# Performance work log

Hardware: AMD Instinct MI355X
Metric: run time of the kernel (lower is better)

Reference implementation:

```python
import jax, jax.numpy as jnp
import numpy as np

N = 50000   # nodes
E = 400000  # edges
F = 128     # in_channels == heads*out_channels (H*C)
H = 8       # heads
C = 16      # per-head out_channels (hidden_channels)
ED = 16     # edge_dim
G = 64      # num graphs in batch
OUT = 64    # encoder out_channels
NEG = 0.2   # leaky_relu negative slope
EPS = 1e-5  # batchnorm eps


def setup_inputs() -> dict:
    key = jax.random.key(0)
    ks = jax.random.split(key, 16)
    s = 0.09  # ~xavier scale for fan_in 128
    return {
        "x": jax.random.normal(ks[0], (N, F), jnp.float32),
        "edge_index": jax.random.randint(ks[1], (2, E), 0, N, dtype=jnp.int32),
        "edge_attr": jax.random.normal(ks[2], (E, ED), jnp.float32),
        "batch": jnp.sort(jax.random.randint(ks[3], (N,), 0, G, dtype=jnp.int32)),
        "lin_qkv": jax.random.normal(ks[4], (3, 3, F, F), jnp.float32) * s,   # [layer, q/k/v, out, in]
        "lin_edge": jax.random.normal(ks[5], (3, F, ED), jnp.float32) * s,    # [layer, out, edge_dim]
        "att": jax.random.normal(ks[6], (3, 3, H, C), jnp.float32) * 0.1,     # [layer, att_q/att_k/att_edge, H, C]
        "gat_bias": jnp.zeros((3, F), jnp.float32),
        "bn_scale": jnp.ones((3, F), jnp.float32),
        "bn_bias": jnp.zeros((3, F), jnp.float32),
        "W1": jax.random.normal(ks[7], (64, 128), jnp.float32) * s,
        "b1": jnp.zeros((64,), jnp.float32),
        "bn1_s": jnp.ones((64,), jnp.float32),
        "bn1_b": jnp.zeros((64,), jnp.float32),
        "W2": jax.random.normal(ks[8], (32, 64), jnp.float32) * 0.12,
        "b2": jnp.zeros((32,), jnp.float32),
        "bn2_s": jnp.ones((32,), jnp.float32),
        "bn2_b": jnp.zeros((32,), jnp.float32),
        "Wout": jax.random.normal(ks[9], (OUT, 32), jnp.float32) * 0.17,
        "bout": jnp.zeros((OUT,), jnp.float32),
    }


def _bn(h, scale, shift):
    # training-mode BatchNorm1d: biased batch statistics (torch default)
    mu = h.mean(axis=0)
    var = h.var(axis=0)
    return (h - mu) * jax.lax.rsqrt(var + EPS) * scale + shift


def reference(x, edge_index, edge_attr, batch, lin_qkv, lin_edge, att, gat_bias,
              bn_scale, bn_bias, W1, b1, bn1_s, bn1_b, W2, b2, bn2_s, bn2_b, Wout, bout):
    src = edge_index[0]  # j (message source)
    dst = edge_index[1]  # i (message target)
    h = x
    for i in range(3):  # fixed num_layers, structurally distinct params
        q = (h @ lin_qkv[i, 0].T).reshape(N, H, C)
        k = (h @ lin_qkv[i, 1].T).reshape(N, H, C)
        v = (h @ lin_qkv[i, 2].T).reshape(N, H, C)
        e = (edge_attr @ lin_edge[i].T).reshape(E, H, C)
        # alpha = q_i*att_q*(k_j*att_k) + edge*att_edge, summed over C  -> [E,H]
        a = (q[dst] * att[i, 0] * (k[src] * att[i, 1]) + e * att[i, 2]).sum(axis=-1)
        a = jnp.where(a > 0, a, NEG * a)  # leaky_relu
        # segment softmax over incoming edges of each target node
        amax = jax.ops.segment_max(a, dst, num_segments=N)
        a = jnp.exp(a - amax[dst])
        a = a / (jax.ops.segment_sum(a, dst, num_segments=N)[dst] + 1e-16)
        out = jax.ops.segment_sum(v[src] * a[:, :, None], dst, num_segments=N)
        out = out.reshape(N, H * C) + gat_bias[i]  # concat heads + bias
        out = _bn(out, bn_scale[i], bn_bias[i])
        if i < 2:
            out = jax.nn.relu(out)  # dropout p=0.2 inactive in eval
        h = out
    g = jax.ops.segment_max(h, batch, num_segments=G)  # global_max_pool [G, H*C]
    z = jax.nn.relu(_bn(g @ W1.T + b1, bn1_s, bn1_b))
    z = jax.nn.relu(_bn(z @ W2.T + b2, bn2_s, bn2_b))
    return z @ Wout.T + bout  # [G, OUT]
```

## Files before the change

### kernel.cpp

```cpp
#include <hip/hip_runtime.h>
#include <hip/hip_bf16.h>
#include <hip/hip_fp16.h>
#include <cstddef>
#include <cstdint>

#define NN 50000
#define EE 400000
#define GG 64
#define MB 391
#define MB2 782

typedef __attribute__((ext_vector_type(8))) _Float16 f16x8;
typedef __attribute__((ext_vector_type(4))) float f32x4;

#define GLOAD_LDS16(g, l) __builtin_amdgcn_global_load_lds( \
    (const __attribute__((address_space(1))) void*)(g), \
    (__attribute__((address_space(3))) void*)(l), 16, 0, 0)

__device__ __forceinline__ unsigned f2key(float f) {
    unsigned u = __float_as_uint(f);
    return (u & 0x80000000u) ? ~u : (u | 0x80000000u);
}
__device__ __forceinline__ float key2f(unsigned k) {
    unsigned u = (k & 0x80000000u) ? (k ^ 0x80000000u) : ~k;
    return __uint_as_float(u);
}

__global__ void compute_M_kernel(const float* __restrict__ lin_edge,
                                 const float* __restrict__ att,
                                 float* __restrict__ M) {
    int t = blockIdx.x * 256 + threadIdx.x;
    if (t >= 3 * 128) return;
    int l = t >> 7, r = t & 127, h = r >> 4, d = r & 15;
    const float* le = lin_edge + (size_t)l * 128 * 16;
    const float* av = att + ((l * 3 + 2) * 128) + h * 16;
    float acc = 0.f;
#pragma unroll
    for (int c = 0; c < 16; ++c) acc += le[(h * 16 + c) * 16 + d] * av[c];
    M[t] = acc;
}

__global__ __launch_bounds__(256)
void wpack_kernel(const float* __restrict__ lin_qkv, __half* __restrict__ Wpack) {
    int g = blockIdx.x * 256 + threadIdx.x;
    int lm = g >> 11;
    int r = g & 2047;
    int kb = r >> 9;
    int kg = (r >> 7) & 3;
    int n  = r & 127;
    int k0 = kb * 32 + kg * 8;
    const float* row = lin_qkv + ((size_t)lm * 128 + n) * 128 + k0;
    __half o[8] __attribute__((aligned(16)));
#pragma unroll
    for (int i = 0; i < 8; ++i) o[i] = __float2half(row[i]);
    *reinterpret_cast<uint4*>(Wpack + (size_t)g * 8) = *reinterpret_cast<const uint4*>(o);
}

__global__ __launch_bounds__(256)
void pack_x_kernel(const float* __restrict__ hin, __half* __restrict__ Apack) {
    int s = blockIdx.x * 256 + threadIdx.x;
    int mb = s >> 11;
    int r  = s & 2047;
    int kb = r >> 9;
    int kg = (r >> 7) & 3;
    int m  = r & 127;
    int node = mb * 128 + m;
    int k0 = kb * 32 + kg * 8;
    size_t slot = ((size_t)(mb * 4 + kb) * 512 + (size_t)kg * 128 + m) * 8;
    __half o[8] __attribute__((aligned(16)));
    if (node < NN) {
        const float* row = hin + (size_t)node * 128 + k0;
#pragma unroll
        for (int i = 0; i < 8; ++i) o[i] = __float2half(row[i]);
    } else {
#pragma unroll
        for (int i = 0; i < 8; ++i) o[i] = __float2half(0.f);
    }
    *reinterpret_cast<uint4*>(Apack + slot) = *reinterpret_cast<const uint4*>(o);
}

__global__ __launch_bounds__(256)
void pack_h_kernel(const __half* __restrict__ hin, const float* __restrict__ sums,
                   const float* __restrict__ scale, const float* __restrict__ shift,
                   __half* __restrict__ Apack) {
    int s = blockIdx.x * 256 + threadIdx.x;
    int mb = s >> 11;
    int r  = s & 2047;
    int kb = r >> 9;
    int kg = (r >> 7) & 3;
    int m  = r & 127;
    int node = mb * 128 + m;
    int k0 = kb * 32 + kg * 8;
    size_t slot = ((size_t)(mb * 4 + kb) * 512 + (size_t)kg * 128 + m) * 8;
    __half o[8] __attribute__((aligned(16)));
    if (node < NN) {
        const __half* row = hin + (size_t)node * 128 + k0;
        uint4 raw = *reinterpret_cast<const uint4*>(row);
        const __half* rh = reinterpret_cast<const __half*>(&raw);
#pragma unroll
        for (int i = 0; i < 8; ++i) {
            int c = k0 + i;
            float mu = sums[c] * (1.f / NN);
            float var = sums[128 + c] * (1.f / NN) - mu * mu;
            float v = (__half2float(rh[i]) - mu) * rsqrtf(var + 1e-5f) * scale[c] + shift[c];
            v = v > 0.f ? v : 0.f;
            o[i] = __float2half(v);
        }
    } else {
#pragma unroll
        for (int i = 0; i < 8; ++i) o[i] = __float2half(0.f);
    }
    *reinterpret_cast<uint4*>(Apack + slot) = *reinterpret_cast<const uint4*>(o);
}

__global__ __launch_bounds__(256, 4)
void qkv_mfma_kernel(const __half* __restrict__ Apack,
                     const __half* __restrict__ Wpack,
                     int layer,
                     const float* __restrict__ att_l,
                     __half* __restrict__ qa, __half* __restrict__ kv) {
    __shared__ __half As[4][2048];
    __shared__ __half Bb[2][4096];
    const int t = threadIdx.x;
    const int lane = t & 63;
    const int wave = t >> 6;
    const int wr = wave >> 1, wc = wave & 1;
    const int r0 = blockIdx.x * 64;
    const int mbk = blockIdx.x >> 1;
    const int half = blockIdx.x & 1;

    const __half* Abase = Apack + (size_t)mbk * 16384;
    const __half* Bl = Wpack + (size_t)layer * 3 * 16384;

#pragma unroll
    for (int kb = 0; kb < 4; ++kb) {
        const __half* ga = Abase + (size_t)kb * 4096 + (size_t)(t >> 6) * 1024 + half * 512 + (size_t)(t & 63) * 8;
        GLOAD_LDS16(ga, &As[kb][((t >> 6) * 64 + (t & 63)) * 8]);
    }
    {
        const __half* gb = Bl + (size_t)t * 8;
        GLOAD_LDS16(gb, &Bb[0][(size_t)t * 8]);
        GLOAD_LDS16(gb + 2048, &Bb[0][2048 + (size_t)t * 8]);
    }
    __syncthreads();

    const int abase = ((lane >> 4) * 64 + wr * 32 + (lane & 15)) * 8;
    const int bbase = ((lane >> 4) * 128 + wc * 64 + (lane & 15)) * 8;
    const int rowq = (lane >> 4) * 4;

    for (int mat = 0; mat < 3; ++mat) {
        f32x4 acc[2][4];
#pragma unroll
        for (int i = 0; i < 2; ++i)
#pragma unroll
            for (int j = 0; j < 4; ++j) acc[i][j] = (f32x4){0.f, 0.f, 0.f, 0.f};

#pragma unroll
        for (int c = 0; c < 4; ++c) {
            int g = mat * 4 + c;
            if (g < 11) {
                const __half* gb = Bl + (size_t)(g + 1) * 4096 + (size_t)t * 8;
                GLOAD_LDS16(gb, &Bb[(g + 1) & 1][(size_t)t * 8]);
                GLOAD_LDS16(gb + 2048, &Bb[(g + 1) & 1][2048 + (size_t)t * 8]);
            }
            f16x8 aF[2], bF[4];
#pragma unroll
            for (int mf = 0; mf < 2; ++mf)
                aF[mf] = *reinterpret_cast<const f16x8*>(&As[c][abase + mf * 128]);
#pragma unroll
            for (int nf = 0; nf < 4; ++nf)
                bF[nf] = *reinterpret_cast<const f16x8*>(&Bb[g & 1][bbase + nf * 128]);
#pragma unroll
            for (int mf = 0; mf < 2; ++mf)
#pragma unroll
                for (int nf = 0; nf < 4; ++nf)
                    acc[mf][nf] = __builtin_amdgcn_mfma_f32_16x16x32_f16(aF[mf], bF[nf], acc[mf][nf], 0, 0, 0);
            __syncthreads();
        }

        __half* outb = (mat == 0) ? qa : kv;
        const size_t stride = (mat == 0) ? 128 : 256;
        const int coloff = (mat == 2) ? 128 : 0;
        float sc[4];
#pragma unroll
        for (int nf = 0; nf < 4; ++nf) {
            int col = wc * 64 + nf * 16 + (lane & 15);
            sc[nf] = (mat == 2) ? 1.f : att_l[mat * 128 + col];
        }
#pragma unroll
        for (int mf = 0; mf < 2; ++mf) {
            int row0 = r0 + wr * 32 + mf * 16 + rowq;
#pragma unroll
            for (int reg = 0; reg < 4; ++reg) {
                int row = row0 + reg;
                if (row < NN) {
#pragma unroll
                    for (int nf = 0; nf < 4; ++nf) {
                        int col = wc * 64 + nf * 16 + (lane & 15);
                        outb[(size_t)row * stride + coloff + col] = __float2half(acc[mf][nf][reg] * sc[nf]);
                    }
                }
            }
        }
    }
}

__global__ __launch_bounds__(256)
void deg_count_kernel(const int* __restrict__ ei, int* __restrict__ deg) {
    int e = blockIdx.x * 256 + threadIdx.x;
    if (e < EE) atomicAdd(&deg[ei[EE + e]], 1);
}

__global__ __launch_bounds__(256)
void scan_partial_kernel(const int* __restrict__ deg, int* __restrict__ psum) {
    __shared__ int red[256];
    int i = blockIdx.x * 256 + threadIdx.x;
    red[threadIdx.x] = (i < NN) ? deg[i] : 0;
    __syncthreads();
    for (int o = 128; o > 0; o >>= 1) {
        if (threadIdx.x < o) red[threadIdx.x] += red[threadIdx.x + o];
        __syncthreads();
    }
    if (threadIdx.x == 0) psum[blockIdx.x] = red[0];
}

__global__ __launch_bounds__(256)
void scan_top_kernel(const int* __restrict__ psum, int* __restrict__ psx) {
    __shared__ int sh[256];
    int t = threadIdx.x;
    int v = (t < 196) ? psum[t] : 0;
    sh[t] = v;
    __syncthreads();
    for (int o = 1; o < 256; o <<= 1) {
        int add = (t >= o) ? sh[t - o] : 0;
        __syncthreads();
        sh[t] += add;
        __syncthreads();
    }
    if (t < 196) psx[t] = sh[t] - v;
}

__global__ __launch_bounds__(256)
void scan_final_kernel(const int* __restrict__ deg, const int* __restrict__ psx,
                       int* __restrict__ offs, int* __restrict__ cursor) {
    __shared__ int sh[256];
    int t = threadIdx.x;
    int i = blockIdx.x * 256 + t;
    int v = (i < NN) ? deg[i] : 0;
    sh[t] = v;
    __syncthreads();
    for (int o = 1; o < 256; o <<= 1) {
        int add = (t >= o) ? sh[t - o] : 0;
        __syncthreads();
        sh[t] += add;
        __syncthreads();
    }
    if (i < NN) {
        int excl = sh[t] - v + psx[blockIdx.x];
        offs[i] = excl;
        cursor[i] = excl;
    }
}

__global__ __launch_bounds__(256)
void scatter_kernel(const int* __restrict__ ei, int* __restrict__ cursor,
                    int2* __restrict__ csr) {
    int e = blockIdx.x * 256 + threadIdx.x;
    if (e < EE) {
        int src = ei[e], dst = ei[EE + e];
        int pos = atomicAdd(&cursor[dst], 1);
        csr[pos] = make_int2(src, e);
    }
}

__global__ __launch_bounds__(256)
void eatt_build_kernel(const float* __restrict__ edge_attr, const int2* __restrict__ csr,
                       const float* __restrict__ M, __half* __restrict__ eatt) {
    __shared__ float Ms[384];
    for (int i = threadIdx.x; i < 384; i += 256) Ms[i] = M[i];
    __syncthreads();
    int pos = blockIdx.x * 256 + threadIdx.x;
    if (pos >= EE) return;
    int e = csr[pos].y;
    const float4* ep = reinterpret_cast<const float4*>(edge_attr + (size_t)e * 16);
    float4 a0 = ep[0], a1 = ep[1], a2 = ep[2], a3 = ep[3];
    float ea[16] = {a0.x, a0.y, a0.z, a0.w, a1.x, a1.y, a1.z, a1.w,
                    a2.x, a2.y, a2.z, a2.w, a3.x, a3.y, a3.z, a3.w};
#pragma unroll
    for (int l = 0; l < 3; ++l) {
        __half o[8] __attribute__((aligned(16)));
#pragma unroll
        for (int h = 0; h < 8; ++h) {
            const float* mp = Ms + l * 128 + h * 16;
            float acc = 0.f;
#pragma unroll
            for (int d = 0; d < 16; ++d) acc += ea[d] * mp[d];
            o[h] = __float2half(acc);
        }
        *reinterpret_cast<uint4*>(eatt + ((size_t)l * EE + pos) * 8) =
            *reinterpret_cast<const uint4*>(o);
    }
}

__global__ __launch_bounds__(128)
void fused_gat_kernel(const __half* __restrict__ qa, const __half* __restrict__ kv,
                      const __half* __restrict__ eatt_l,
                      const int* __restrict__ offs, const int* __restrict__ deg,
                      const int2* __restrict__ csr, __half* __restrict__ hout) {
    int lane = threadIdx.x & 63;
    int n = blockIdx.x * 2 + (threadIdx.x >> 6);
    if (n >= NN) return;
    int h = lane >> 3;
    int c2h = lane & 7;
    int chh = h * 8 + c2h;

    float2 q = __half22float2(reinterpret_cast<const __half2*>(qa + (size_t)n * 128)[chh]);

    int start = offs[n], d = deg[n];
    const __half* ebase = eatt_l + (size_t)start * 8 + h;
    const int2* cbase = csr + start;

    float den = 0.f, acc0 = 0.f, acc1 = 0.f;
    int i = 0;
    for (; i + 8 <= d; i += 8) {
        int s[8]; float e[8]; __half2 kh[8], vh[8];
#pragma unroll
        for (int j = 0; j < 8; ++j) s[j] = cbase[i + j].x;
#pragma unroll
        for (int j = 0; j < 8; ++j) e[j] = __half2float(ebase[(size_t)(i + j) * 8]);
#pragma unroll
        for (int j = 0; j < 8; ++j) {
            const __half2* ph = reinterpret_cast<const __half2*>(kv + (size_t)s[j] * 256);
            kh[j] = ph[chh];
            vh[j] = ph[64 + chh];
        }
#pragma unroll
        for (int j = 0; j < 8; ++j) {
            float2 k = __half22float2(kh[j]);
            float p = q.x * k.x + q.y * k.y;
            p += __shfl_xor(p, 1); p += __shfl_xor(p, 2); p += __shfl_xor(p, 4);
            float a = p + e[j]; a = a > 0.f ? a : 0.2f * a;
            a = fminf(a, 60.f);
            float w = __expf(a);
            float2 v = __half22float2(vh[j]);
            den += w; acc0 += w * v.x; acc1 += w * v.y;
        }
    }
    for (; i + 4 <= d; i += 4) {
        int s[4]; float e[4]; __half2 kh[4], vh[4];
#pragma unroll
        for (int j = 0; j < 4; ++j) s[j] = cbase[i + j].x;
#pragma unroll
        for (int j = 0; j < 4; ++j) e[j] = __half2float(ebase[(size_t)(i + j) * 8]);
#pragma unroll
        for (int j = 0; j < 4; ++j) {
            const __half2* ph = reinterpret_cast<const __half2*>(kv + (size_t)s[j] * 256);
            kh[j] = ph[chh];
            vh[j] = ph[64 + chh];
        }
#pragma unroll
        for (int j = 0; j < 4; ++j) {
            float2 k = __half22float2(kh[j]);
            float p = q.x * k.x + q.y * k.y;
            p += __shfl_xor(p, 1); p += __shfl_xor(p, 2); p += __shfl_xor(p, 4);
            float a = p + e[j]; a = a > 0.f ? a : 0.2f * a;
            a = fminf(a, 60.f);
            float w = __expf(a);
            float2 v = __half22float2(vh[j]);
            den += w; acc0 += w * v.x; acc1 += w * v.y;
        }
    }
    for (; i < d; ++i) {
        int s0 = cbase[i].x;
        float e0 = __half2float(ebase[(size_t)i * 8]);
        const __half2* ph = reinterpret_cast<const __half2*>(kv + (size_t)s0 * 256);
        float2 k = __half22float2(ph[chh]);
        float2 v = __half22float2(ph[64 + chh]);
        float p = q.x * k.x + q.y * k.y;
        p += __shfl_xor(p, 1); p += __shfl_xor(p, 2); p += __shfl_xor(p, 4);
        float a = p + e0; a = a > 0.f ? a : 0.2f * a;
        a = fminf(a, 60.f);
        float w = __expf(a);
        den += w; acc0 += w * v.x; acc1 += w * v.y;
    }
    float inv = 1.f / (den + 1e-16f);
    reinterpret_cast<__half2*>(hout + (size_t)n * 128)[chh] =
        __float22half2_rn(make_float2(acc0 * inv, acc1 * inv));
}

__global__ __launch_bounds__(256)
void bn_stats_kernel(const __half* __restrict__ h, float* __restrict__ sums) {
    __shared__ float red[2][16][128];
    int t = threadIdx.x;
    int cg = t & 15;
    int rofs = t >> 4;
    int r0 = blockIdx.x * 64;
    int rend = min(NN, r0 + 64);
    float s1[8], s2[8];
#pragma unroll
    for (int j = 0; j < 8; ++j) { s1[j] = 0.f; s2[j] = 0.f; }
    for (int r = r0 + rofs; r < rend; r += 16) {
        uint4 raw = *reinterpret_cast<const uint4*>(h + (size_t)r * 128 + cg * 8);
        const __half* rh = reinterpret_cast<const __half*>(&raw);
#pragma unroll
        for (int j = 0; j < 8; ++j) {
            float v = __half2float(rh[j]);
            s1[j] += v; s2[j] += v * v;
        }
    }
#pragma unroll
    for (int j = 0; j < 8; ++j) {
        red[0][rofs][cg * 8 + j] = s1[j];
        red[1][rofs][cg * 8 + j] = s2[j];
    }
    __syncthreads();
    if (t < 128) {
        float a = 0.f, b = 0.f;
#pragma unroll
        for (int i = 0; i < 16; ++i) { a += red[0][i][t]; b += red[1][i][t]; }
        unsafeAtomicAdd(&sums[t], a);
        unsafeAtomicAdd(&sums[128 + t], b);
    }
}

__global__ __launch_bounds__(256)
void bn_pool_kernel(const __half* __restrict__ h, const float* __restrict__ sums,
                    const float* __restrict__ scale, const float* __restrict__ shift,
                    const int* __restrict__ batch, unsigned* __restrict__ gkey) {
    int t = threadIdx.x;
    int c = t & 127, half = t >> 7;
    int r0 = blockIdx.x * 32;
    int rend = min(NN, r0 + 32);
    const float invN = 1.f / (float)NN;
    float mu = sums[c] * invN;
    float var = sums[128 + c] * invN - mu * mu;
    float iscl = rsqrtf(var + 1e-5f) * scale[c];
    float sh = shift[c];
    int curg = -1;
    float lmax = -INFINITY;
    for (int r = r0 + half; r < rend; r += 2) {
        int g = batch[r];
        if (g != curg) {
            if (curg >= 0) atomicMax(&gkey[curg * 128 + c], f2key(lmax));
            curg = g;
            lmax = -INFINITY;
        }
        float v = (__half2float(h[(size_t)r * 128 + c]) - mu) * iscl + sh;
        lmax = fmaxf(lmax, v);
    }
    if (curg >= 0) atomicMax(&gkey[curg * 128 + c], f2key(lmax));
}

__global__ __launch_bounds__(256)
void head_kernel(const unsigned* __restrict__ gkey,
                 const float* __restrict__ W1, const float* __restrict__ b1,
                 const float* __restrict__ bn1s, const float* __restrict__ bn1b,
                 const float* __restrict__ W2, const float* __restrict__ b2,
                 const float* __restrict__ bn2s, const float* __restrict__ bn2b,
                 const float* __restrict__ Wout, const float* __restrict__ bout,
                 float* __restrict__ out) {
    __shared__ float g[64][128];
    __shared__ float z1[64][64];
    __shared__ float z2[64][32];
    int t = threadIdx.x;
    for (int i = t; i < 64 * 128; i += 256) g[i >> 7][i & 127] = key2f(gkey[i]);
    __syncthreads();
    for (int i = t; i < 64 * 64; i += 256) {
        int r = i >> 6, o = i & 63;
        const float* gr = g[r];
        const float* wr = W1 + (size_t)o * 128;
        float acc = b1[o];
        for (int k2 = 0; k2 < 128; ++k2) acc += gr[k2] * wr[k2];
        z1[r][o] = acc;
    }
    __syncthreads();
    if (t < 64) {
        float s1 = 0.f, s2 = 0.f;
        for (int r = 0; r < 64; ++r) { float v = z1[r][t]; s1 += v; s2 += v * v; }
        float mu = s1 * (1.f / 64.f), var = s2 * (1.f / 64.f) - mu * mu;
        float inv = rsqrtf(var + 1e-5f) * bn1s[t];
        float sh = bn1b[t];
        for (int r = 0; r < 64; ++r) {
            float v = (z1[r][t] - mu) * inv + sh;
            z1[r][t] = v > 0.f ? v : 0.f;
        }
    }
    __syncthreads();
    for (int i = t; i < 64 * 32; i += 256) {
        int r = i >> 5, o = i & 31;
        const float* wr = W2 + (size_t)o * 64;
        float acc = b2[o];
        for (int k2 = 0; k2 < 64; ++k2) acc += z1[r][k2] * wr[k2];
        z2[r][o] = acc;
    }
    __syncthreads();
    if (t < 32) {
        float s1 = 0.f, s2 = 0.f;
        for (int r = 0; r < 64; ++r) { float v = z2[r][t]; s1 += v; s2 += v * v; }
        float mu = s1 * (1.f / 64.f), var = s2 * (1.f / 64.f) - mu * mu;
        float inv = rsqrtf(var + 1e-5f) * bn2s[t];
        float sh = bn2b[t];
        for (int r = 0; r < 64; ++r) {
            float v = (z2[r][t] - mu) * inv + sh;
            z2[r][t] = v > 0.f ? v : 0.f;
        }
    }
    __syncthreads();
    for (int i = t; i < 64 * 64; i += 256) {
        int r = i >> 6, o = i & 63;
        const float* wr = Wout + (size_t)o * 32;
        float acc = bout[o];
        for (int k2 = 0; k2 < 32; ++k2) acc += z2[r][k2] * wr[k2];
        out[r * 64 + o] = acc;
    }
}

extern "C" void kernel_launch(void* const* d_in, const int* in_sizes, int n_in,
                              void* d_out, int out_size, void* d_ws, size_t ws_size,
                              hipStream_t stream) {
    const float* x         = (const float*)d_in[0];
    const int*   ei        = (const int*)d_in[1];
    const float* edge_attr = (const float*)d_in[2];
    const int*   batch     = (const int*)d_in[3];
    const float* lin_qkv   = (const float*)d_in[4];
    const float* lin_edge  = (const float*)d_in[5];
    const float* att       = (const float*)d_in[6];
    const float* bn_scale  = (const float*)d_in[8];
    const float* bn_bias   = (const float*)d_in[9];
    const float* W1   = (const float*)d_in[10];
    const float* b1   = (const float*)d_in[11];
    const float* bn1s = (const float*)d_in[12];
    const float* bn1b = (const float*)d_in[13];
    const float* W2   = (const float*)d_in[14];
    const float* b2   = (const float*)d_in[15];
    const float* bn2s = (const float*)d_in[16];
    const float* bn2b = (const float*)d_in[17];
    const float* Wout = (const float*)d_in[18];
    const float* bout = (const float*)d_in[19];

    float* ws = (float*)d_ws;
    size_t off = 0;
    auto alloc = [&](size_t n) { float* p = ws + off; off += n; return p; };
    int*      deg   = (int*)alloc(NN);
    unsigned* gkey  = (unsigned*)alloc(64 * 128);
    float*    gsums = alloc(3 * 256);
    const size_t zeroBytes = ((size_t)NN + 64 * 128 + 3 * 256) * 4;
    __half* hout = (__half*)alloc((size_t)NN * 64);
    __half* qa   = (__half*)alloc((size_t)NN * 64);
    __half* kv   = (__half*)alloc((size_t)NN * 128);
    __half* Apack = (__half*)alloc((size_t)MB * 8192);
    __half* Wpack = (__half*)alloc(9 * 8192);
    int*    offs   = (int*)alloc(NN);
    int*    cursor = (int*)alloc(NN);
    int2*   csr    = (int2*)alloc((size_t)EE * 2);
    __half* eatt   = (__half*)alloc((size_t)3 * EE * 4);
    int*    psum   = (int*)alloc(256);
    int*    psx    = (int*)alloc(256);
    float*  M      = alloc(3 * 128);

    const int edgeBlocks = (EE + 255) / 256;
    const int scanBlocks = (NN + 255) / 256;
    const int packBlocks = MB * 8;
    const int statBlocks = (NN + 63) / 64;
    const int poolBlocks = (NN + 31) / 32;
    const int gatBlocks  = (NN + 1) / 2;

    hipMemsetAsync(deg, 0, zeroBytes, stream);
    wpack_kernel<<<72, 256, 0, stream>>>(lin_qkv, Wpack);
    compute_M_kernel<<<2, 256, 0, stream>>>(lin_edge, att, M);
    deg_count_kernel<<<edgeBlocks, 256, 0, stream>>>(ei, deg);
    scan_partial_kernel<<<scanBlocks, 256, 0, stream>>>(deg, psum);
    scan_top_kernel<<<1, 256, 0, stream>>>(psum, psx);
    scan_final_kernel<<<scanBlocks, 256, 0, stream>>>(deg, psx, offs, cursor);
    scatter_kernel<<<edgeBlocks, 256, 0, stream>>>(ei, cursor, csr);
    eatt_build_kernel<<<edgeBlocks, 256, 0, stream>>>(edge_attr, csr, M, eatt);
    pack_x_kernel<<<packBlocks, 256, 0, stream>>>(x, Apack);

    for (int l = 0; l < 3; ++l) {
        qkv_mfma_kernel<<<MB2, 256, 0, stream>>>(
            Apack, Wpack, l, att + (size_t)l * 384, qa, kv);

        fused_gat_kernel<<<gatBlocks, 128, 0, stream>>>(
            qa, kv, eatt + (size_t)l * EE * 8, offs, deg, csr, hout);

        bn_stats_kernel<<<statBlocks, 256, 0, stream>>>(hout, gsums + l * 256);

        if (l < 2) {
            pack_h_kernel<<<packBlocks, 256, 0, stream>>>(
                hout, gsums + l * 256, bn_scale + l * 128, bn_bias + l * 128, Apack);
        } else {
            bn_pool_kernel<<<poolBlocks, 256, 0, stream>>>(
                hout, gsums + l * 256, bn_scale + l * 128, bn_bias + l * 128, batch, gkey);
        }
    }

    head_kernel<<<1, 256, 0, stream>>>(gkey, W1, b1, bn1s, bn1b, W2, b2, bn2s, bn2b, Wout, bout, (float*)d_out);
}
```

Before: 387.0 us.

## Merge prologue kernels, fold scan top into final, retune stats/eatt and head MLP

Combines weight packing, edge-attention matrix and input packing into one prologue launch. Folds the single-block scan_top into scan_final, so each block reduces the preceding partial sums itself. Has each thread build two edges in eatt_build, halves the rows per bn_stats block, and stages W1 and the pooled features as fp16 in shared memory for the head MLP. The aim is fewer launches and better utilisation, at the cost of fp16 rounding in the first MLP layer and redundant per-block reductions in the scan.

```diff
diff --git a/kernel.cpp b/kernel.cpp
--- a/kernel.cpp
+++ b/kernel.cpp
@@ -26,57 +26,57 @@
     return __uint_as_float(u);
 }
 
-__global__ void compute_M_kernel(const float* __restrict__ lin_edge,
-                                 const float* __restrict__ att,
-                                 float* __restrict__ M) {
-    int t = blockIdx.x * 256 + threadIdx.x;
-    if (t >= 3 * 128) return;
-    int l = t >> 7, r = t & 127, h = r >> 4, d = r & 15;
-    const float* le = lin_edge + (size_t)l * 128 * 16;
-    const float* av = att + ((l * 3 + 2) * 128) + h * 16;
-    float acc = 0.f;
-#pragma unroll
-    for (int c = 0; c < 16; ++c) acc += le[(h * 16 + c) * 16 + d] * av[c];
-    M[t] = acc;
-}
-
-__global__ __launch_bounds__(256)
-void wpack_kernel(const float* __restrict__ lin_qkv, __half* __restrict__ Wpack) {
-    int g = blockIdx.x * 256 + threadIdx.x;
-    int lm = g >> 11;
-    int r = g & 2047;
-    int kb = r >> 9;
-    int kg = (r >> 7) & 3;
-    int n  = r & 127;
-    int k0 = kb * 32 + kg * 8;
-    const float* row = lin_qkv + ((size_t)lm * 128 + n) * 128 + k0;
-    __half o[8] __attribute__((aligned(16)));
-#pragma unroll
-    for (int i = 0; i < 8; ++i) o[i] = __float2half(row[i]);
-    *reinterpret_cast<uint4*>(Wpack + (size_t)g * 8) = *reinterpret_cast<const uint4*>(o);
-}
-
-__global__ __launch_bounds__(256)
-void pack_x_kernel(const float* __restrict__ hin, __half* __restrict__ Apack) {
-    int s = blockIdx.x * 256 + threadIdx.x;
-    int mb = s >> 11;
-    int r  = s & 2047;
-    int kb = r >> 9;
-    int kg = (r >> 7) & 3;
-    int m  = r & 127;
-    int node = mb * 128 + m;
-    int k0 = kb * 32 + kg * 8;
-    size_t slot = ((size_t)(mb * 4 + kb) * 512 + (size_t)kg * 128 + m) * 8;
-    __half o[8] __attribute__((aligned(16)));
-    if (node < NN) {
-        const float* row = hin + (size_t)node * 128 + k0;
+__global__ __launch_bounds__(256)
+void prologue_kernel(const float* __restrict__ lin_qkv, const float* __restrict__ lin_edge,
+                     const float* __restrict__ att, const float* __restrict__ x,
+                     __half* __restrict__ Wpack, float* __restrict__ M,
+                     __half* __restrict__ Apack) {
+    int b = blockIdx.x;
+    int t = threadIdx.x;
+    if (b < 72) {
+        int g = b * 256 + t;
+        int lm = g >> 11;
+        int r = g & 2047;
+        int kb = r >> 9;
+        int kg = (r >> 7) & 3;
+        int n  = r & 127;
+        int k0 = kb * 32 + kg * 8;
+        const float* row = lin_qkv + ((size_t)lm * 128 + n) * 128 + k0;
+        __half o[8] __attribute__((aligned(16)));
 #pragma unroll
         for (int i = 0; i < 8; ++i) o[i] = __float2half(row[i]);
+        *reinterpret_cast<uint4*>(Wpack + (size_t)g * 8) = *reinterpret_cast<const uint4*>(o);
+    } else if (b < 74) {
+        int g = (b - 72) * 256 + t;
+        if (g >= 3 * 128) return;
+        int l = g >> 7, r = g & 127, h = r >> 4, d = r & 15;
+        const float* le = lin_edge + (size_t)l * 128 * 16;
+        const float* av = att + ((l * 3 + 2) * 128) + h * 16;
+        float acc = 0.f;
+#pragma unroll
+        for (int c = 0; c < 16; ++c) acc += le[(h * 16 + c) * 16 + d] * av[c];
+        M[g] = acc;
     } else {
-#pragma unroll
-        for (int i = 0; i < 8; ++i) o[i] = __float2half(0.f);
-    }
-    *reinterpret_cast<uint4*>(Apack + slot) = *reinterpret_cast<const uint4*>(o);
+        int s = (b - 74) * 256 + t;
+        int mb = s >> 11;
+        int r  = s & 2047;
+        int kb = r >> 9;
+        int kg = (r >> 7) & 3;
+        int m  = r & 127;
+        int node = mb * 128 + m;
+        int k0 = kb * 32 + kg * 8;
+        size_t slot = ((size_t)(mb * 4 + kb) * 512 + (size_t)kg * 128 + m) * 8;
+        __half o[8] __attribute__((aligned(16)));
+        if (node < NN) {
+            const float* row = x + (size_t)node * 128 + k0;
+#pragma unroll
+            for (int i = 0; i < 8; ++i) o[i] = __float2half(row[i]);
+        } else {
+#pragma unroll
+            for (int i = 0; i < 8; ++i) o[i] = __float2half(0.f);
+        }
+        *reinterpret_cast<uint4*>(Apack + slot) = *reinterpret_cast<const uint4*>(o);
+    }
 }
 
 __global__ __launch_bounds__(256)
@@ -225,10 +225,21 @@
 }
 
 __global__ __launch_bounds__(256)
-void scan_top_kernel(const int* __restrict__ psum, int* __restrict__ psx) {
+void scan_final_kernel(const int* __restrict__ deg, const int* __restrict__ psum,
+                       int* __restrict__ offs, int* __restrict__ cursor) {
+    __shared__ int red[256];
     __shared__ int sh[256];
     int t = threadIdx.x;
-    int v = (t < 196) ? psum[t] : 0;
+    int b = blockIdx.x;
+    red[t] = (t < b) ? psum[t] : 0;
+    __syncthreads();
+    for (int o = 128; o > 0; o >>= 1) {
+        if (t < o) red[t] += red[t + o];
+        __syncthreads();
+    }
+    int base = red[0];
+    int i = b * 256 + t;
+    int v = (i < NN) ? deg[i] : 0;
     sh[t] = v;
     __syncthreads();
     for (int o = 1; o < 256; o <<= 1) {
@@ -237,26 +248,8 @@
         sh[t] += add;
         __syncthreads();
     }
-    if (t < 196) psx[t] = sh[t] - v;
-}
-
-__global__ __launch_bounds__(256)
-void scan_final_kernel(const int* __restrict__ deg, const int* __restrict__ psx,
-                       int* __restrict__ offs, int* __restrict__ cursor) {
-    __shared__ int sh[256];
-    int t = threadIdx.x;
-    int i = blockIdx.x * 256 + t;
-    int v = (i < NN) ? deg[i] : 0;
-    sh[t] = v;
-    __syncthreads();
-    for (int o = 1; o < 256; o <<= 1) {
-        int add = (t >= o) ? sh[t - o] : 0;
-        __syncthreads();
-        sh[t] += add;
-        __syncthreads();
-    }
     if (i < NN) {
-        int excl = sh[t] - v + psx[blockIdx.x];
+        int excl = sh[t] - v + base;
         offs[i] = excl;
         cursor[i] = excl;
     }
@@ -279,26 +272,30 @@
     __shared__ float Ms[384];
     for (int i = threadIdx.x; i < 384; i += 256) Ms[i] = M[i];
     __syncthreads();
-    int pos = blockIdx.x * 256 + threadIdx.x;
-    if (pos >= EE) return;
-    int e = csr[pos].y;
-    const float4* ep = reinterpret_cast<const float4*>(edge_attr + (size_t)e * 16);
-    float4 a0 = ep[0], a1 = ep[1], a2 = ep[2], a3 = ep[3];
-    float ea[16] = {a0.x, a0.y, a0.z, a0.w, a1.x, a1.y, a1.z, a1.w,
-                    a2.x, a2.y, a2.z, a2.w, a3.x, a3.y, a3.z, a3.w};
-#pragma unroll
-    for (int l = 0; l < 3; ++l) {
-        __half o[8] __attribute__((aligned(16)));
-#pragma unroll
-        for (int h = 0; h < 8; ++h) {
-            const float* mp = Ms + l * 128 + h * 16;
-            float acc = 0.f;
-#pragma unroll
-            for (int d = 0; d < 16; ++d) acc += ea[d] * mp[d];
-            o[h] = __float2half(acc);
-        }
-        *reinterpret_cast<uint4*>(eatt + ((size_t)l * EE + pos) * 8) =
-            *reinterpret_cast<const uint4*>(o);
+    int pos0 = (blockIdx.x * 256 + threadIdx.x) * 2;
+#pragma unroll
+    for (int u = 0; u < 2; ++u) {
+        int pos = pos0 + u;
+        if (pos >= EE) return;
+        int e = csr[pos].y;
+        const float4* ep = reinterpret_cast<const float4*>(edge_attr + (size_t)e * 16);
+        float4 a0 = ep[0], a1 = ep[1], a2 = ep[2], a3 = ep[3];
+        float ea[16] = {a0.x, a0.y, a0.z, a0.w, a1.x, a1.y, a1.z, a1.w,
+                        a2.x, a2.y, a2.z, a2.w, a3.x, a3.y, a3.z, a3.w};
+#pragma unroll
+        for (int l = 0; l < 3; ++l) {
+            __half o[8] __attribute__((aligned(16)));
+#pragma unroll
+            for (int h = 0; h < 8; ++h) {
+                const float* mp = Ms + l * 128 + h * 16;
+                float acc = 0.f;
+#pragma unroll
+                for (int d = 0; d < 16; ++d) acc += ea[d] * mp[d];
+                o[h] = __float2half(acc);
+            }
+            *reinterpret_cast<uint4*>(eatt + ((size_t)l * EE + pos) * 8) =
+                *reinterpret_cast<const uint4*>(o);
+        }
     }
 }
 
@@ -394,8 +391,8 @@
     int t = threadIdx.x;
     int cg = t & 15;
     int rofs = t >> 4;
-    int r0 = blockIdx.x * 64;
-    int rend = min(NN, r0 + 64);
+    int r0 = blockIdx.x * 32;
+    int rend = min(NN, r0 + 32);
     float s1[8], s2[8];
 #pragma unroll
     for (int j = 0; j < 8; ++j) { s1[j] = 0.f; s2[j] = 0.f; }
@@ -459,18 +456,20 @@
                  const float* __restrict__ bn2s, const float* __restrict__ bn2b,
                  const float* __restrict__ Wout, const float* __restrict__ bout,
                  float* __restrict__ out) {
-    __shared__ float g[64][128];
+    __shared__ __half gh[64][128];
+    __shared__ __half W1s[64][130];
     __shared__ float z1[64][64];
     __shared__ float z2[64][32];
     int t = threadIdx.x;
-    for (int i = t; i < 64 * 128; i += 256) g[i >> 7][i & 127] = key2f(gkey[i]);
+    for (int i = t; i < 64 * 128; i += 256) gh[i >> 7][i & 127] = __float2half(key2f(gkey[i]));
+    for (int i = t; i < 64 * 128; i += 256) W1s[i >> 7][i & 127] = __float2half(W1[i]);
     __syncthreads();
     for (int i = t; i < 64 * 64; i += 256) {
         int r = i >> 6, o = i & 63;
-        const float* gr = g[r];
-        const float* wr = W1 + (size_t)o * 128;
         float acc = b1[o];
-        for (int k2 = 0; k2 < 128; ++k2) acc += gr[k2] * wr[k2];
+#pragma unroll 8
+        for (int k2 = 0; k2 < 128; ++k2)
+            acc += __half2float(gh[r][k2]) * __half2float(W1s[o][k2]);
         z1[r][o] = acc;
     }
     __syncthreads();
@@ -555,26 +554,23 @@
     int2*   csr    = (int2*)alloc((size_t)EE * 2);
     __half* eatt   = (__half*)alloc((size_t)3 * EE * 4);
     int*    psum   = (int*)alloc(256);
-    int*    psx    = (int*)alloc(256);
     float*  M      = alloc(3 * 128);
 
     const int edgeBlocks = (EE + 255) / 256;
     const int scanBlocks = (NN + 255) / 256;
     const int packBlocks = MB * 8;
-    const int statBlocks = (NN + 63) / 64;
+    const int statBlocks = (NN + 31) / 32;
     const int poolBlocks = (NN + 31) / 32;
     const int gatBlocks  = (NN + 1) / 2;
+    const int eattBlocks = (EE + 511) / 512;
 
     hipMemsetAsync(deg, 0, zeroBytes, stream);
-    wpack_kernel<<<72, 256, 0, stream>>>(lin_qkv, Wpack);
-    compute_M_kernel<<<2, 256, 0, stream>>>(lin_edge, att, M);
+    prologue_kernel<<<74 + packBlocks, 256, 0, stream>>>(lin_qkv, lin_edge, att, x, Wpack, M, Apack);
     deg_count_kernel<<<edgeBlocks, 256, 0, stream>>>(ei, deg);
     scan_partial_kernel<<<scanBlocks, 256, 0, stream>>>(deg, psum);
-    scan_top_kernel<<<1, 256, 0, stream>>>(psum, psx);
-    scan_final_kernel<<<scanBlocks, 256, 0, stream>>>(deg, psx, offs, cursor);
+    scan_final_kernel<<<scanBlocks, 256, 0, stream>>>(deg, psum, offs, cursor);
     scatter_kernel<<<edgeBlocks, 256, 0, stream>>>(ei, cursor, csr);
-    eatt_build_kernel<<<edgeBlocks, 256, 0, stream>>>(edge_attr, csr, M, eatt);
-    pack_x_kernel<<<packBlocks, 256, 0, stream>>>(x, Apack);
+    eatt_build_kernel<<<eattBlocks, 256, 0, stream>>>(edge_attr, csr, M, eatt);
 
     for (int l = 0; l < 3; ++l) {
         qkv_mfma_kernel<<<MB2, 256, 0, stream>>>(
```

New measurement: 440.6 us. 1.14x slower.
